# Optimization experiments

Measured on AMD Instinct MI355X. Metric: run time of the kernel, lower is better.

Reference implementation:

```python
import jax, jax.numpy as jnp
import numpy as np

B, L, D_IN, H, N2, NL = 8, 4096, 128, 256, 8, 4  # d_state=16 -> N2=8 conjugate pairs


def setup_inputs() -> dict:
    key = jax.random.key(0)
    ks = jax.random.split(key, 10)
    x = jax.random.normal(ks[0], (B, L, D_IN), jnp.float32)
    enc_w = jax.random.normal(ks[1], (H, D_IN), jnp.float32) / np.float32(np.sqrt(D_IN))
    enc_b = jax.random.normal(ks[2], (H,), jnp.float32) * 0.01
    # S4D kernel params, stacked over NL layers
    log_dt = (jax.random.uniform(ks[3], (NL, H), jnp.float32)
              * np.float32(np.log(0.1) - np.log(0.001)) + np.float32(np.log(0.001)))
    log_A_real = jnp.full((NL, H, N2), np.float32(np.log(0.5)), jnp.float32)
    A_imag = jnp.ones((NL, H, 1), jnp.float32) * (np.pi * jnp.arange(N2, dtype=jnp.float32))
    C_re = jax.random.normal(ks[4], (NL, H, N2), jnp.float32) * np.float32(0.5 ** 0.5)
    C_im = jax.random.normal(ks[5], (NL, H, N2), jnp.float32) * np.float32(0.5 ** 0.5)
    D_skip = jax.random.normal(ks[6], (NL, H), jnp.float32)
    out_w = jax.random.normal(ks[7], (NL, 2 * H, H), jnp.float32) / np.float32(np.sqrt(H))
    out_b = jnp.zeros((NL, 2 * H), jnp.float32)
    return {"x": x, "enc_w": enc_w, "enc_b": enc_b, "log_dt": log_dt,
            "log_A_real": log_A_real, "A_imag": A_imag, "C_re": C_re, "C_im": C_im,
            "D_skip": D_skip, "out_w": out_w, "out_b": out_b}


def _s4d_layer(z, log_dt, log_A_real, A_imag, C_re, C_im, D_skip, out_w, out_b):
    # z: (B, L, H) -> u: (B, H, L)
    u = jnp.swapaxes(z, 1, 2)
    Lq = u.shape[-1]
    dt = jnp.exp(log_dt)                       # (H,)
    A = -jnp.exp(log_A_real) + 1j * A_imag     # (H, N2) complex
    dtA = A * dt[:, None]                      # (H, N2)
    Ck = (C_re + 1j * C_im) * (jnp.exp(dtA) - 1.0) / A  # ZOH discretization of C
    # Vandermonde kernel: K[h,l] = 2*Re(sum_n Ck[h,n] * exp(dtA[h,n]*l))
    t = jnp.arange(Lq, dtype=jnp.float32)
    K = 2.0 * jnp.einsum('hn,hnl->hl', Ck, jnp.exp(dtA[:, :, None] * t)).real  # (H, L)
    # FFT circular conv on 2L grid -> causal linear conv
    n_fft = 2 * Lq
    y = jnp.fft.irfft(jnp.fft.rfft(u, n=n_fft) * jnp.fft.rfft(K, n=n_fft), n=n_fft)[..., :Lq]
    y = y + u * D_skip[:, None]                # skip connection
    y = jax.nn.gelu(y)                         # final_act='gelu'
    y = jnp.einsum('bhl,ph->bpl', y, out_w) + out_b[None, :, None]  # 1x1 conv H->2H
    a, g = jnp.split(y, 2, axis=1)
    y = a * jax.nn.sigmoid(g)                  # GLU
    return jnp.swapaxes(y, 1, 2)               # (B, L, H)


def reference(x, enc_w, enc_b, log_dt, log_A_real, A_imag, C_re, C_im, D_skip, out_w, out_b):
    h = x @ enc_w.T + enc_b                    # encoder Linear: (B, L, H)
    for i in range(NL):                        # small fixed structural loop over layers
        z = _s4d_layer(h, log_dt[i], log_A_real[i], A_imag[i],
                       C_re[i], C_im[i], D_skip[i], out_w[i], out_b[i])
        h = z + h                              # residual (dropout=0 -> identity)
    return h
```

## Files before the change

kernel.cpp:

```cpp
#include <hip/hip_runtime.h>
#include <hip/hip_bf16.h>
#include <math.h>

#define Bn   8
#define Ln   4096
#define DINn 128
#define Hn   256
#define N2n  8
#define NLn  4
#define NP   4

typedef __attribute__((ext_vector_type(4))) float f32x4;
typedef __attribute__((ext_vector_type(2))) float f32x2;
typedef __attribute__((ext_vector_type(8))) short bf16x8;

__device__ __forceinline__ float gelu_f(float x) {
    float x2 = x * x;
    float inner = 0.7978845608028654f * x * fmaf(0.044715f, x2, 1.0f);
    float e = __expf(2.0f * inner);
    float th = 1.0f - 2.0f / (e + 1.0f);
    return 0.5f * x * (1.0f + th);
}

__device__ __forceinline__ float sigmoid_f(float x) {
    return 1.0f / (1.0f + __expf(-x));
}

__device__ __forceinline__ unsigned short f2bf(float f) {
    union { __hip_bfloat16 b; unsigned short u; } cv;
    cv.b = __float2bfloat16(f);
    return cv.u;
}

__device__ __forceinline__ uint4 pack8(float4 a, float4 b) {
    uint4 v;
    v.x = (unsigned)f2bf(a.x) | ((unsigned)f2bf(a.y) << 16);
    v.y = (unsigned)f2bf(a.z) | ((unsigned)f2bf(a.w) << 16);
    v.z = (unsigned)f2bf(b.x) | ((unsigned)f2bf(b.y) << 16);
    v.w = (unsigned)f2bf(b.z) | ((unsigned)f2bf(b.w) << 16);
    return v;
}

#define PKFMA(a, b, c) __builtin_elementwise_fma((f32x2)(a), (f32x2)(b), (f32x2)(c))

__global__ __launch_bounds__(256) void s4_scan_kernel(
    const float* __restrict__ hT,
    unsigned short* __restrict__ yT,
    const float* __restrict__ log_dt,
    const float* __restrict__ log_A_real,
    const float* __restrict__ A_imag,
    const float* __restrict__ C_re,
    const float* __restrict__ C_im,
    const float* __restrict__ D_skip)
{
    __shared__ float u_lds[4][64][65];
    const int tid = threadIdx.x;
    const int v = tid >> 6;
    const int t = tid & 63;
    const int h = blockIdx.x * 4 + v;
    const int b = blockIdx.y;

    const size_t rowbase = (size_t)(b * Hn + h) * Ln + (size_t)t * 64;
    const float* src = hT + rowbase;
    float* uL = &u_lds[v][t][0];

    #pragma unroll
    for (int j4 = 0; j4 < 16; ++j4) {
        float4 g = *(const float4*)(src + j4 * 4);
        uL[j4 * 4 + 0] = g.x; uL[j4 * 4 + 1] = g.y;
        uL[j4 * 4 + 2] = g.z; uL[j4 * 4 + 3] = g.w;
    }

    float dt = expf(log_dt[h]);
    f32x2 wrp[NP], wip[NP], crp[NP], cip[NP];
    #pragma unroll
    for (int q = 0; q < NP; ++q) {
        #pragma unroll
        for (int e = 0; e < 2; ++e) {
            int n = 2 * q + e;
            float lar = log_A_real[h * N2n + n];
            float aim = A_imag[h * N2n + n];
            float are = -expf(lar);
            float mag = expf(are * dt);
            float s_, c_;
            sincosf(aim * dt, &s_, &c_);
            float w_re = mag * c_, w_im = mag * s_;
            float nre = w_re - 1.0f, nim = w_im;
            float inv = 1.0f / (are * are + aim * aim);
            float tre = (nre * are + nim * aim) * inv;
            float tim = (nim * are - nre * aim) * inv;
            float Cr = C_re[h * N2n + n], Ci = C_im[h * N2n + n];
            wrp[q][e] = w_re; wip[q][e] = w_im;
            crp[q][e] = Cr * tre - Ci * tim;
            cip[q][e] = Cr * tim + Ci * tre;
        }
    }
    const float Dsk = D_skip[h];

    f32x2 srp[NP], sip[NP];
    #pragma unroll
    for (int q = 0; q < NP; ++q) { srp[q] = (f32x2)0.0f; sip[q] = (f32x2)0.0f; }
    #pragma unroll 4
    for (int j = 0; j < 64; ++j) {
        float u = uL[j];
        f32x2 uu = { u, u };
        #pragma unroll
        for (int q = 0; q < NP; ++q) {
            f32x2 nr = PKFMA(wrp[q], srp[q], PKFMA(-wip[q], sip[q], uu));
            f32x2 ni = PKFMA(wip[q], srp[q], wrp[q] * sip[q]);
            srp[q] = nr; sip[q] = ni;
        }
    }

    f32x2 mrp[NP], mip[NP];
    #pragma unroll
    for (int q = 0; q < NP; ++q) {
        f32x2 ar = wrp[q], ai = wip[q];
        #pragma unroll
        for (int s = 0; s < 6; ++s) {
            f32x2 nr2 = ar * ar - ai * ai;
            ai = 2.0f * ar * ai;
            ar = nr2;
        }
        mrp[q] = ar; mip[q] = ai;
    }
    for (int dlt = 1; dlt < 64; dlt <<= 1) {
        #pragma unroll
        for (int q = 0; q < NP; ++q) {
            f32x2 tr, ti;
            tr.x = __shfl_up(srp[q].x, (unsigned)dlt, 64);
            tr.y = __shfl_up(srp[q].y, (unsigned)dlt, 64);
            ti.x = __shfl_up(sip[q].x, (unsigned)dlt, 64);
            ti.y = __shfl_up(sip[q].y, (unsigned)dlt, 64);
            f32x2 trz = (t >= dlt) ? tr : (f32x2)0.0f;
            f32x2 tiz = (t >= dlt) ? ti : (f32x2)0.0f;
            srp[q] = PKFMA(mrp[q], trz, PKFMA(-mip[q], tiz, srp[q]));
            sip[q] = PKFMA(mrp[q], tiz, PKFMA(mip[q], trz, sip[q]));
        }
        #pragma unroll
        for (int q = 0; q < NP; ++q) {
            f32x2 nr2 = mrp[q] * mrp[q] - mip[q] * mip[q];
            mip[q] = 2.0f * mrp[q] * mip[q];
            mrp[q] = nr2;
        }
    }
    #pragma unroll
    for (int q = 0; q < NP; ++q) {
        f32x2 er, ei;
        er.x = __shfl_up(srp[q].x, 1u, 64);
        er.y = __shfl_up(srp[q].y, 1u, 64);
        ei.x = __shfl_up(sip[q].x, 1u, 64);
        ei.y = __shfl_up(sip[q].y, 1u, 64);
        srp[q] = (t >= 1) ? er : (f32x2)0.0f;
        sip[q] = (t >= 1) ? ei : (f32x2)0.0f;
    }

    unsigned short* dst = yT + rowbase;
    for (int j8 = 0; j8 < 8; ++j8) {
        unsigned short rs[8];
        #pragma unroll
        for (int c = 0; c < 8; ++c) {
            float u = uL[j8 * 8 + c];
            f32x2 uu = { u, u };
            f32x2 accp = (f32x2)0.0f;
            #pragma unroll
            for (int q = 0; q < NP; ++q) {
                f32x2 nr = PKFMA(wrp[q], srp[q], PKFMA(-wip[q], sip[q], uu));
                f32x2 ni = PKFMA(wip[q], srp[q], wrp[q] * sip[q]);
                srp[q] = nr; sip[q] = ni;
                accp = PKFMA(crp[q], nr, PKFMA(-cip[q], ni, accp));
            }
            float acc = accp.x + accp.y;
            float yv = fmaf(2.0f, acc, Dsk * u);
            rs[c] = f2bf(gelu_f(yv));
        }
        uint4 o;
        o.x = (unsigned)rs[0] | ((unsigned)rs[1] << 16);
        o.y = (unsigned)rs[2] | ((unsigned)rs[3] << 16);
        o.z = (unsigned)rs[4] | ((unsigned)rs[5] << 16);
        o.w = (unsigned)rs[6] | ((unsigned)rs[7] << 16);
        *(uint4*)(dst + j8 * 8) = o;
    }
}

template<int KDIM, bool GLU, bool ACVT, bool KMAJ, bool LAST>
__global__ __launch_bounds__(256) void mfma_gemm(
    const unsigned short* __restrict__ Abf,
    const float* __restrict__ Af,
    const float* __restrict__ W,
    const float* __restrict__ ba,
    const float* __restrict__ bg,
    float* hTbuf,
    float* Hout)
{
    constexpr int SM_MAIN = 128 * 72 * 2 + (GLU ? 2 : 1) * 64 * 72 * 2;
    constexpr int SM_TS = 64 * 132 * 4;
    constexpr int SM = SM_MAIN > SM_TS ? SM_MAIN : SM_TS;
    __shared__ __align__(16) char smem[SM];
    unsigned short* As  = (unsigned short*)smem;
    unsigned short* Bs0 = As + 128 * 72;
    unsigned short* Bs1 = Bs0 + 64 * 72;
    float* ts = (float*)smem;

    const int tid = threadIdx.x;
    const int lane = tid & 63, w = tid >> 6;
    const int wm = w >> 1, wn = w & 1;
    const int lr = lane & 15, lq = lane >> 4;
    const int row0 = blockIdx.x * 128;
    const int n0 = blockIdx.y * 64;
    const int bb = row0 >> 12;
    const int l0 = row0 & (Ln - 1);

    f32x4 accA[4][2], accG[4][2];
    #pragma unroll
    for (int i = 0; i < 4; ++i)
        #pragma unroll
        for (int j = 0; j < 2; ++j) {
            accA[i][j] = (f32x4)0.0f;
            if constexpr (GLU) accG[i][j] = (f32x4)0.0f;
        }

    for (int kt = 0; kt < KDIM / 64; ++kt) {
        const int k0 = kt * 64;
        if constexpr (ACVT) {
            #pragma unroll
            for (int it = 0; it < 4; ++it) {
                int idx = it * 256 + tid; int m = idx >> 3, q = idx & 7;
                const float* s = Af + (size_t)(row0 + m) * KDIM + k0 + q * 8;
                float4 g1 = *(const float4*)s;
                float4 g2 = *(const float4*)(s + 4);
                *(uint4*)(&As[m * 72 + q * 8]) = pack8(g1, g2);
            }
        } else {
            #pragma unroll
            for (int it = 0; it < 4; ++it) {
                int p = tid >> 2;
                int c = (tid & 3) | (it << 2);
                uint4 g = *(const uint4*)(Abf + (size_t)(bb * Hn + k0 + p) * Ln + l0 + c * 8);
                unsigned short* d = &As[(c * 8) * 72 + p];
                d[0 * 72] = g.x & 0xffff; d[1 * 72] = g.x >> 16;
                d[2 * 72] = g.y & 0xffff; d[3 * 72] = g.y >> 16;
                d[4 * 72] = g.z & 0xffff; d[5 * 72] = g.z >> 16;
                d[6 * 72] = g.w & 0xffff; d[7 * 72] = g.w >> 16;
            }
        }
        #pragma unroll
        for (int it = 0; it < 2; ++it) {
            int idx = it * 256 + tid; int p = idx >> 3, q = idx & 7;
            {
                const float* s = W + (size_t)(n0 + p) * KDIM + k0 + q * 8;
                float4 g1 = *(const float4*)s;
                float4 g2 = *(const float4*)(s + 4);
                *(uint4*)(&Bs0[p * 72 + q * 8]) = pack8(g1, g2);
            }
            if constexpr (GLU) {
                const float* s = W + (size_t)(256 + n0 + p) * KDIM + k0 + q * 8;
                float4 g1 = *(const float4*)s;
                float4 g2 = *(const float4*)(s + 4);
                *(uint4*)(&Bs1[p * 72 + q * 8]) = pack8(g1, g2);
            }
        }
        __syncthreads();
        #pragma unroll
        for (int kf = 0; kf < 2; ++kf) {
            bf16x8 av[4], bv[2], gv[2];
            #pragma unroll
            for (int mf = 0; mf < 4; ++mf)
                av[mf] = *(const bf16x8*)(&As[(wm * 64 + mf * 16 + lr) * 72 + (kf * 4 + lq) * 8]);
            #pragma unroll
            for (int nf = 0; nf < 2; ++nf) {
                bv[nf] = *(const bf16x8*)(&Bs0[(wn * 32 + nf * 16 + lr) * 72 + (kf * 4 + lq) * 8]);
                if constexpr (GLU)
                    gv[nf] = *(const bf16x8*)(&Bs1[(wn * 32 + nf * 16 + lr) * 72 + (kf * 4 + lq) * 8]);
            }
            #pragma unroll
            for (int mf = 0; mf < 4; ++mf)
                #pragma unroll
                for (int nf = 0; nf < 2; ++nf) {
                    accA[mf][nf] = __builtin_amdgcn_mfma_f32_16x16x32_bf16(av[mf], bv[nf], accA[mf][nf], 0, 0, 0);
                    if constexpr (GLU)
                        accG[mf][nf] = __builtin_amdgcn_mfma_f32_16x16x32_bf16(av[mf], gv[nf], accG[mf][nf], 0, 0, 0);
                }
        }
        __syncthreads();
    }

    float bA[2], bG[2];
    #pragma unroll
    for (int nf = 0; nf < 2; ++nf) {
        int pc = n0 + wn * 32 + nf * 16 + lr;
        bA[nf] = ba[pc];
        if constexpr (GLU) bG[nf] = bg[pc];
    }
    #pragma unroll
    for (int mf = 0; mf < 4; ++mf) {
        #pragma unroll
        for (int r = 0; r < 4; ++r) {
            int m_loc = wm * 64 + mf * 16 + lq * 4 + r;
            #pragma unroll
            for (int nf = 0; nf < 2; ++nf) {
                float val;
                if constexpr (GLU) {
                    float aval = accA[mf][nf][r] + bA[nf];
                    float gval = accG[mf][nf][r] + bG[nf];
                    val = aval * sigmoid_f(gval);
                } else {
                    val = accA[mf][nf][r] + bA[nf];
                }
                ts[(wn * 32 + nf * 16 + lr) * 132 + m_loc] = val;
            }
        }
    }
    __syncthreads();

    if constexpr (!LAST) {
        #pragma unroll
        for (int it2 = 0; it2 < 8; ++it2) {
            int idx = it2 * 256 + tid;
            int nn = idx >> 5, m4 = (idx & 31) * 4;
            float4 o = *(const float4*)(&ts[nn * 132 + m4]);
            float* gp = hTbuf + (size_t)(bb * Hn + n0 + nn) * Ln + l0 + m4;
            if constexpr (GLU) {
                float4 rr = *(const float4*)gp;
                o.x += rr.x; o.y += rr.y; o.z += rr.z; o.w += rr.w;
            }
            *(float4*)gp = o;
        }
    } else {
        #pragma unroll
        for (int it2 = 0; it2 < 8; ++it2) {
            int idx = it2 * 256 + tid;
            int nn = idx >> 5, m4 = (idx & 31) * 4;
            float4 o = *(const float4*)(&ts[nn * 132 + m4]);
            const float* gp = hTbuf + (size_t)(bb * Hn + n0 + nn) * Ln + l0 + m4;
            float4 rr = *(const float4*)gp;
            o.x += rr.x; o.y += rr.y; o.z += rr.z; o.w += rr.w;
            *(float4*)(&ts[nn * 132 + m4]) = o;
        }
        __syncthreads();
        #pragma unroll
        for (int it2 = 0; it2 < 8; ++it2) {
            int idx = it2 * 256 + tid;
            int m = idx >> 4, n4 = (idx & 15) * 4;
            float4 o;
            o.x = ts[(n4 + 0) * 132 + m];
            o.y = ts[(n4 + 1) * 132 + m];
            o.z = ts[(n4 + 2) * 132 + m];
            o.w = ts[(n4 + 3) * 132 + m];
            *(float4*)(Hout + (size_t)(row0 + m) * Hn + n0 + n4) = o;
        }
    }
}

extern "C" void kernel_launch(void* const* d_in, const int* in_sizes, int n_in,
                              void* d_out, int out_size, void* d_ws, size_t ws_size,
                              hipStream_t stream) {
    (void)in_sizes; (void)n_in; (void)out_size; (void)ws_size;
    const float* x          = (const float*)d_in[0];
    const float* enc_w      = (const float*)d_in[1];
    const float* enc_b      = (const float*)d_in[2];
    const float* log_dt     = (const float*)d_in[3];
    const float* log_A_real = (const float*)d_in[4];
    const float* A_imag     = (const float*)d_in[5];
    const float* C_re       = (const float*)d_in[6];
    const float* C_im       = (const float*)d_in[7];
    const float* D_skip     = (const float*)d_in[8];
    const float* out_w      = (const float*)d_in[9];
    const float* out_b      = (const float*)d_in[10];

    const size_t NE = (size_t)Bn * Hn * Ln;
    float* h  = (float*)d_out;
    float* hT = (float*)d_ws;
    unsigned short* yT = (unsigned short*)(hT + NE);

    const dim3 gg(256, 4), gb(256);

    mfma_gemm<DINn, false, true, false, false><<<gg, gb, 0, stream>>>(
        nullptr, x, enc_w, enc_b, nullptr, hT, nullptr);

    for (int i = 0; i < NLn; ++i) {
        s4_scan_kernel<<<dim3(Hn / 4, Bn), gb, 0, stream>>>(
            hT, yT,
            log_dt + (size_t)i * Hn,
            log_A_real + (size_t)i * Hn * N2n,
            A_imag + (size_t)i * Hn * N2n,
            C_re + (size_t)i * Hn * N2n,
            C_im + (size_t)i * Hn * N2n,
            D_skip + (size_t)i * Hn);
        const float* wlay = out_w + (size_t)i * 2 * Hn * Hn;
        const float* bl = out_b + (size_t)i * 2 * Hn;
        if (i == NLn - 1) {
            mfma_gemm<Hn, true, false, true, true><<<gg, gb, 0, stream>>>(
                yT, nullptr, wlay, bl, bl + Hn, hT, h);
        } else {
            mfma_gemm<Hn, true, false, true, false><<<gg, gb, 0, stream>>>(
                yT, nullptr, wlay, bl, bl + Hn, hT, nullptr);
        }
    }
}
```

Measured before the change: 257.7 us.

## Split each S4 scan row across two waves and stage I/O through LDS

The scan kernel now handles each (batch, channel) row with two waves of 64 threads, each thread owning 32 steps instead of 64. The first half's end state is passed to the second half through shared memory and applied with a per-lane power of the decay. This doubles the number of blocks and halves the serial recurrence length per thread. Inputs are loaded with coalesced float4 reads into a padded LDS tile, and outputs are written back from LDS in coalesced bf16 packs. The costs are extra barriers and possibly misaligned 128-bit LDS accesses, since rows are padded to a stride of 33 floats.

```diff
diff --git a/kernel.cpp b/kernel.cpp
--- a/kernel.cpp
+++ b/kernel.cpp
@@ -43,7 +43,7 @@
 
 #define PKFMA(a, b, c) __builtin_elementwise_fma((f32x2)(a), (f32x2)(b), (f32x2)(c))
 
-__global__ __launch_bounds__(256) void s4_scan_kernel(
+__global__ __launch_bounds__(256, 4) void s4_scan_kernel(
     const float* __restrict__ hT,
     unsigned short* __restrict__ yT,
     const float* __restrict__ log_dt,
@@ -53,23 +53,30 @@
     const float* __restrict__ C_im,
     const float* __restrict__ D_skip)
 {
-    __shared__ float u_lds[4][64][65];
+    __shared__ float uC[2 * 128 * 33];
+    __shared__ float Sbuf[2][16];
+
     const int tid = threadIdx.x;
-    const int v = tid >> 6;
+    const int w = tid >> 6;
     const int t = tid & 63;
-    const int h = blockIdx.x * 4 + v;
+    const int rowloc = w >> 1;
+    const int half = w & 1;
+    const int h = blockIdx.x * 2 + rowloc;
     const int b = blockIdx.y;
 
-    const size_t rowbase = (size_t)(b * Hn + h) * Ln + (size_t)t * 64;
-    const float* src = hT + rowbase;
-    float* uL = &u_lds[v][t][0];
-
-    #pragma unroll
-    for (int j4 = 0; j4 < 16; ++j4) {
-        float4 g = *(const float4*)(src + j4 * 4);
-        uL[j4 * 4 + 0] = g.x; uL[j4 * 4 + 1] = g.y;
-        uL[j4 * 4 + 2] = g.z; uL[j4 * 4 + 3] = g.w;
-    }
+    const float* gsrc = hT + (size_t)(b * Hn + blockIdx.x * 2) * Ln;
+    #pragma unroll
+    for (int it = 0; it < 8; ++it) {
+        int idx4 = it * 256 + tid;
+        float4 g = *(const float4*)(gsrc + (size_t)idx4 * 4);
+        int e = idx4 * 4;
+        int r = e >> 12, ep = e & 4095;
+        int c = ep >> 5, off = ep & 31;
+        *(float4*)(&uC[(r * 128 + c) * 33 + off]) = g;
+    }
+    __syncthreads();
+
+    float* uL = &uC[(rowloc * 128 + half * 64 + t) * 33];
 
     float dt = expf(log_dt[h]);
     f32x2 wrp[NP], wip[NP], crp[NP], cip[NP];
@@ -101,7 +108,7 @@
     #pragma unroll
     for (int q = 0; q < NP; ++q) { srp[q] = (f32x2)0.0f; sip[q] = (f32x2)0.0f; }
     #pragma unroll 4
-    for (int j = 0; j < 64; ++j) {
+    for (int j = 0; j < 32; ++j) {
         float u = uL[j];
         f32x2 uu = { u, u };
         #pragma unroll
@@ -112,18 +119,20 @@
         }
     }
 
-    f32x2 mrp[NP], mip[NP];
+    f32x2 mrp[NP], mip[NP], arp[NP], aip[NP];
     #pragma unroll
     for (int q = 0; q < NP; ++q) {
         f32x2 ar = wrp[q], ai = wip[q];
         #pragma unroll
-        for (int s = 0; s < 6; ++s) {
+        for (int s = 0; s < 5; ++s) {
             f32x2 nr2 = ar * ar - ai * ai;
             ai = 2.0f * ar * ai;
             ar = nr2;
         }
         mrp[q] = ar; mip[q] = ai;
-    }
+        arp[q] = (f32x2)1.0f; aip[q] = (f32x2)0.0f;
+    }
+    #pragma unroll
     for (int dlt = 1; dlt < 64; dlt <<= 1) {
         #pragma unroll
         for (int q = 0; q < NP; ++q) {
@@ -136,12 +145,24 @@
             f32x2 tiz = (t >= dlt) ? ti : (f32x2)0.0f;
             srp[q] = PKFMA(mrp[q], trz, PKFMA(-mip[q], tiz, srp[q]));
             sip[q] = PKFMA(mrp[q], tiz, PKFMA(mip[q], trz, sip[q]));
-        }
-        #pragma unroll
-        for (int q = 0; q < NP; ++q) {
+            f32x2 nar = arp[q] * mrp[q] - aip[q] * mip[q];
+            f32x2 nai = PKFMA(arp[q], mip[q], aip[q] * mrp[q]);
+            bool bit = (t & dlt) != 0;
+            arp[q] = bit ? nar : arp[q];
+            aip[q] = bit ? nai : aip[q];
             f32x2 nr2 = mrp[q] * mrp[q] - mip[q] * mip[q];
             mip[q] = 2.0f * mrp[q] * mip[q];
             mrp[q] = nr2;
+        }
+    }
+
+    if (half == 0 && t == 63) {
+        #pragma unroll
+        for (int q = 0; q < NP; ++q) {
+            Sbuf[rowloc][4 * q + 0] = srp[q].x;
+            Sbuf[rowloc][4 * q + 1] = sip[q].x;
+            Sbuf[rowloc][4 * q + 2] = srp[q].y;
+            Sbuf[rowloc][4 * q + 3] = sip[q].y;
         }
     }
     #pragma unroll
@@ -154,32 +175,46 @@
         srp[q] = (t >= 1) ? er : (f32x2)0.0f;
         sip[q] = (t >= 1) ? ei : (f32x2)0.0f;
     }
-
-    unsigned short* dst = yT + rowbase;
-    for (int j8 = 0; j8 < 8; ++j8) {
-        unsigned short rs[8];
-        #pragma unroll
-        for (int c = 0; c < 8; ++c) {
-            float u = uL[j8 * 8 + c];
-            f32x2 uu = { u, u };
-            f32x2 accp = (f32x2)0.0f;
-            #pragma unroll
-            for (int q = 0; q < NP; ++q) {
-                f32x2 nr = PKFMA(wrp[q], srp[q], PKFMA(-wip[q], sip[q], uu));
-                f32x2 ni = PKFMA(wip[q], srp[q], wrp[q] * sip[q]);
-                srp[q] = nr; sip[q] = ni;
-                accp = PKFMA(crp[q], nr, PKFMA(-cip[q], ni, accp));
-            }
-            float acc = accp.x + accp.y;
-            float yv = fmaf(2.0f, acc, Dsk * u);
-            rs[c] = f2bf(gelu_f(yv));
-        }
-        uint4 o;
-        o.x = (unsigned)rs[0] | ((unsigned)rs[1] << 16);
-        o.y = (unsigned)rs[2] | ((unsigned)rs[3] << 16);
-        o.z = (unsigned)rs[4] | ((unsigned)rs[5] << 16);
-        o.w = (unsigned)rs[6] | ((unsigned)rs[7] << 16);
-        *(uint4*)(dst + j8 * 8) = o;
+    __syncthreads();
+    if (half == 1) {
+        #pragma unroll
+        for (int q = 0; q < NP; ++q) {
+            f32x2 SAr = { Sbuf[rowloc][4 * q + 0], Sbuf[rowloc][4 * q + 2] };
+            f32x2 SAi = { Sbuf[rowloc][4 * q + 1], Sbuf[rowloc][4 * q + 3] };
+            srp[q] = PKFMA(arp[q], SAr, PKFMA(-aip[q], SAi, srp[q]));
+            sip[q] = PKFMA(arp[q], SAi, PKFMA(aip[q], SAr, sip[q]));
+        }
+    }
+
+    #pragma unroll 4
+    for (int j = 0; j < 32; ++j) {
+        float u = uL[j];
+        f32x2 uu = { u, u };
+        f32x2 accp = (f32x2)0.0f;
+        #pragma unroll
+        for (int q = 0; q < NP; ++q) {
+            f32x2 nr = PKFMA(wrp[q], srp[q], PKFMA(-wip[q], sip[q], uu));
+            f32x2 ni = PKFMA(wip[q], srp[q], wrp[q] * sip[q]);
+            srp[q] = nr; sip[q] = ni;
+            accp = PKFMA(crp[q], nr, PKFMA(-cip[q], ni, accp));
+        }
+        float acc = accp.x + accp.y;
+        float yv = fmaf(2.0f, acc, Dsk * u);
+        uL[j] = gelu_f(yv);
+    }
+    __syncthreads();
+
+    unsigned short* gdst = yT + (size_t)(b * Hn + blockIdx.x * 2) * Ln;
+    #pragma unroll
+    for (int it = 0; it < 4; ++it) {
+        int idx8 = it * 256 + tid;
+        int e = idx8 * 8;
+        int r = e >> 12, ep = e & 4095;
+        int c = ep >> 5, off = ep & 31;
+        const float* p = &uC[(r * 128 + c) * 33 + off];
+        float4 ga = *(const float4*)p;
+        float4 gb = *(const float4*)(p + 4);
+        *(uint4*)(gdst + e) = pack8(ga, gb);
     }
 }
 
@@ -379,7 +414,7 @@
         nullptr, x, enc_w, enc_b, nullptr, hT, nullptr);
 
     for (int i = 0; i < NLn; ++i) {
-        s4_scan_kernel<<<dim3(Hn / 4, Bn), gb, 0, stream>>>(
+        s4_scan_kernel<<<dim3(Hn / 2, Bn), gb, 0, stream>>>(
             hT, yT,
             log_dt + (size_t)i * Hn,
             log_A_real + (size_t)i * Hn * N2n,
```

Measured after the change: 304.6 us. +18.2%, slower.
